# Performance work log

Measured on AMD Instinct MI355X. Metric: run time of the kernel, lower is better.

The kernel has to match this reference:

```python
import jax, jax.numpy as jnp
import numpy as np

D = 1024          # d_model
E = 12            # n_routed
HS = 2 * D        # shared hidden (r_shared=2)
HR = 3 * D        # routed hidden (r_routed=3)
TAU = 1.5         # router temperature


def setup_inputs() -> dict:
    key = jax.random.key(0)
    ks = jax.random.split(key, 12)
    def xavier(k, shape):
        fan_in, fan_out = shape[-2], shape[-1]
        lim = jnp.sqrt(6.0 / (fan_in + fan_out))
        return jax.random.uniform(k, shape, jnp.float32, -lim, lim)
    x = jax.random.normal(ks[0], (2, 1024, D), jnp.float32)
    # shared expert (n_shared=1, GEGLU)
    Ws1 = xavier(ks[1], (D, 2 * HS)); bs1 = jnp.zeros((2 * HS,), jnp.float32)
    Ws2 = xavier(ks[2], (HS, D));     bs2 = jnp.zeros((D,), jnp.float32)
    # routed experts, stacked [E, ...]
    We1 = xavier(ks[3], (E, D, 2 * HR)); be1 = jnp.zeros((E, 2 * HR), jnp.float32)
    We2 = xavier(ks[4], (E, HR, D));     be2 = jnp.zeros((E, D), jnp.float32)
    # router
    Wr = xavier(ks[5], (D, E)); br = jnp.zeros((E,), jnp.float32)
    return {"x": x, "Ws1": Ws1, "bs1": bs1, "Ws2": Ws2, "bs2": bs2,
            "We1": We1, "be1": be1, "We2": We2, "be2": be2, "Wr": Wr, "br": br}


def _geglu(h):
    a, g = jnp.split(h, 2, axis=-1)
    return a * jax.nn.gelu(g, approximate=False)  # torch GELU is exact erf


def reference(x, Ws1, bs1, Ws2, bs2, We1, be1, We2, be2, Wr, br):
    B, T, Dm = x.shape
    xf = x.reshape(-1, Dm)                                   # [N, D]
    # shared expert (n_shared=1 -> divide by 1)
    ys = _geglu(xf @ Ws1 + bs1) @ Ws2 + bs2                  # [N, D]
    # top-2 router (eval: no noise)
    logits = (xf @ Wr + br) / TAU                            # [N, E]
    top_val, top_idx = jax.lax.top_k(logits, 2)              # [N, 2]
    top_w = jax.nn.softmax(top_val, axis=-1)                 # [N, 2]
    # combine weights per (token, expert); non-selected experts get 0
    onehot = jax.nn.one_hot(top_idx, E, dtype=x.dtype)       # [N, 2, E]
    w = jnp.einsum('nke,nk->ne', onehot, top_w)              # [N, E]
    # dropless dense dispatch: every expert sees all tokens, weight 0 masks
    h = jnp.einsum('nd,edh->enh', xf, We1) + be1[:, None, :] # [E, N, 2*HR]
    act = _geglu(h)                                          # [E, N, HR]
    yE = jnp.einsum('enh,ehd->end', act, We2) + be2[:, None, :]
    yr = jnp.einsum('end,ne->nd', yE, w)                     # [N, D]
    return (ys + yr).reshape(B, T, Dm)
```

## Files before the change

### kernel.cpp

```cpp
#include <hip/hip_runtime.h>

#define N_TOK 2048
#define DMODEL 1024
#define NEXP 12
#define HS_DIM 2048
#define HR_DIM 3072
#define NSLOT (2 * N_TOK)

typedef __attribute__((ext_vector_type(8))) short bf16x8;
typedef __attribute__((ext_vector_type(16))) float f32x16;

#define AS1 __attribute__((address_space(1)))
#define AS3 __attribute__((address_space(3)))

__device__ __forceinline__ void gl_lds16(const void* g, void* l) {
  __builtin_amdgcn_global_load_lds((const AS1 void*)g, (AS3 void*)l, 16, 0, 0);
}

__device__ __forceinline__ unsigned short f2bf(float x) {
  union { float f; unsigned int u; } v; v.f = x;
  unsigned int u = v.u;
  u += 0x7fff + ((u >> 16) & 1);
  return (unsigned short)(u >> 16);
}
__device__ __forceinline__ unsigned pack2(float a, float b) {
  return (unsigned)f2bf(a) | ((unsigned)f2bf(b) << 16);
}
__device__ __forceinline__ float gelu_exact(float x) {
  return 0.5f * x * (1.0f + erff(x * 0.70710678118654752f));
}


__global__ __launch_bounds__(256)
void convert_x_kernel(const float* __restrict__ X, unsigned short* __restrict__ XB) {
  const int idx = (blockIdx.x * 256 + threadIdx.x) * 8;
  float4 f0 = *(const float4*)(X + idx);
  float4 f1 = *(const float4*)(X + idx + 4);
  uint4 o;
  o.x = pack2(f0.x, f0.y); o.y = pack2(f0.z, f0.w);
  o.z = pack2(f1.x, f1.y); o.w = pack2(f1.z, f1.w);
  *(uint4*)(XB + idx) = o;
}

__global__ __launch_bounds__(256)
void tconv_kernel(const float* __restrict__ W, unsigned short* __restrict__ WT,
                  int K, int N) {
  const int n0 = blockIdx.x * 64;
  const int k0 = blockIdx.y * 64;
  const size_t bo = (size_t)blockIdx.z * K * N;
  __shared__ __align__(16) unsigned short Ts[64 * 72];
  const int t = threadIdx.x;
  const int k4 = (t >> 4) * 4, n4 = (t & 15) * 4;
  float4 rw[4];
#pragma unroll
  for (int i = 0; i < 4; ++i)
    rw[i] = *(const float4*)(W + bo + (size_t)(k0 + k4 + i) * N + n0 + n4);
#pragma unroll
  for (int j = 0; j < 4; ++j) {
    uint2 v;
    v.x = pack2(((const float*)&rw[0])[j], ((const float*)&rw[1])[j]);
    v.y = pack2(((const float*)&rw[2])[j], ((const float*)&rw[3])[j]);
    *(uint2*)&Ts[(n4 + j) * 72 + k4] = v;
  }
  __syncthreads();
  const int n = t >> 2, kc = (t & 3) * 16;
  uint4 v0 = *(const uint4*)&Ts[n * 72 + kc];
  uint4 v1 = *(const uint4*)&Ts[n * 72 + kc + 8];
  unsigned short* dst = WT + (size_t)blockIdx.z * N * K + (size_t)(n0 + n) * K + k0 + kc;
  *(uint4*)dst = v0;
  *(uint4*)(dst + 8) = v1;
}


__global__ void init_kernel(int* counts, int* cursors) {
  int t = threadIdx.x;
  if (t < NEXP) { counts[t] = 0; cursors[t] = 0; }
}

__global__ __launch_bounds__(256)
void router_kernel(const float* __restrict__ X, const float* __restrict__ Wr,
                   const float* __restrict__ br, int* __restrict__ top_e,
                   float* __restrict__ top_w, int* __restrict__ counts) {
  const int wv = threadIdx.x >> 6, lane = threadIdx.x & 63;
  const int n = blockIdx.x * 4 + wv;
  float a[NEXP];
#pragma unroll
  for (int e = 0; e < NEXP; ++e) a[e] = 0.f;
  for (int it = 0; it < DMODEL / 64; ++it) {
    int k = it * 64 + lane;
    float xv = X[(size_t)n * DMODEL + k];
    const float* wr = Wr + (size_t)k * NEXP;
#pragma unroll
    for (int e = 0; e < NEXP; ++e) a[e] += xv * wr[e];
  }
#pragma unroll
  for (int e = 0; e < NEXP; ++e)
    for (int o = 32; o > 0; o >>= 1) a[e] += __shfl_xor(a[e], o, 64);
  if (lane == 0) {
    float l[NEXP];
#pragma unroll
    for (int e = 0; e < NEXP; ++e) l[e] = (a[e] + br[e]) * (1.0f / 1.5f);
    int e0 = 0;
    for (int e = 1; e < NEXP; ++e) if (l[e] > l[e0]) e0 = e;
    int e1 = (e0 == 0) ? 1 : 0;
    for (int e = 0; e < NEXP; ++e) if (e != e0 && l[e] > l[e1]) e1 = e;
    float w0 = 1.f / (1.f + expf(l[e1] - l[e0]));
    top_e[n * 2 + 0] = e0; top_e[n * 2 + 1] = e1;
    top_w[n * 2 + 0] = w0; top_w[n * 2 + 1] = 1.f - w0;
    atomicAdd(&counts[e0], 1); atomicAdd(&counts[e1], 1);
  }
}

__global__ void scan_kernel(const int* __restrict__ counts, int* __restrict__ offs) {
  if (threadIdx.x == 0) {
    int s = 0;
    for (int e = 0; e < NEXP; ++e) { offs[e] = s; s += counts[e]; }
    offs[NEXP] = s;
  }
}

__global__ __launch_bounds__(256)
void fill_kernel(const int* __restrict__ top_e, const float* __restrict__ top_w,
                 const int* __restrict__ offs, int* __restrict__ cursors,
                 int* __restrict__ slot_tok, float* __restrict__ slot_w,
                 int* __restrict__ tok_slot) {
  int n = blockIdx.x * 256 + threadIdx.x;
  if (n >= N_TOK) return;
#pragma unroll
  for (int j = 0; j < 2; ++j) {
    int e = top_e[n * 2 + j];
    int p = atomicAdd(&cursors[e], 1);
    int s = offs[e] + p;
    slot_tok[s] = n;
    slot_w[s] = top_w[n * 2 + j];
    tok_slot[n * 2 + j] = s;
  }
}

#define G1_SHARED 256
#define G1_PER_E  384

__global__ __launch_bounds__(256, 2)
void gemm1_all_kernel(const unsigned short* __restrict__ XB,
                      const unsigned short* __restrict__ WS,
                      const unsigned short* __restrict__ WE,
                      const float* __restrict__ BSb, const float* __restrict__ BEb,
                      unsigned short* __restrict__ ACT_S, unsigned short* __restrict__ ACT_R,
                      const int* __restrict__ slot_tok, const int* __restrict__ offs,
                      const int* __restrict__ counts) {
  int id = blockIdx.x;
  const unsigned short* W; const float* bias; unsigned short* ACT;
  int H, count, off, m0, n0, routed;
  if (id < G1_SHARED) {
    routed = 0;
    m0 = (id >> 4) * 128; n0 = (id & 15) * 128;
    W = WS; bias = BSb; ACT = ACT_S; H = HS_DIM; count = N_TOK; off = 0;
  } else {
    routed = 1;
    id -= G1_SHARED;
    const int e = id / G1_PER_E, rem = id % G1_PER_E;
    m0 = (rem / 24) * 128; n0 = (rem % 24) * 128;
    W = WE + (size_t)e * 2 * HR_DIM * DMODEL;
    bias = BEb + (size_t)e * 2 * HR_DIM;
    ACT = ACT_R; H = HR_DIM; count = counts[e]; off = offs[e];
  }
  if (m0 >= count) return;

  __shared__ __align__(16) unsigned short As[2 * 4096];
  __shared__ __align__(16) unsigned short Bs[2 * 8192];

  const int t = threadIdx.x;
  const int lane = t & 63, wv = t >> 6;
  const int srow = t >> 2, skc = t & 3;
  const int ln31 = lane & 31, hi = lane >> 5;
  const int wr = wv >> 1, wc = wv & 1;
  const int skc_s = skc ^ ((srow >> 1) & 3);

  const unsigned short* ap[2];
#pragma unroll
  for (int g = 0; g < 2; ++g) {
    int mr = m0 + srow + 64 * g;
    int tok;
    if (routed) {
      int s = off + (mr < count ? mr : count - 1);
      tok = slot_tok[s];
    } else {
      tok = mr;
    }
    ap[g] = XB + (size_t)tok * DMODEL + skc_s * 8;
  }
  const unsigned short* bp[4];
#pragma unroll
  for (int g = 0; g < 4; ++g) {
    int brow = srow + 64 * g;
    int wrow = (brow < 128) ? (n0 + brow) : (H + n0 + brow - 128);
    bp[g] = W + (size_t)wrow * DMODEL + skc_s * 8;
  }

  f32x16 acc_a[2][2], acc_g[2][2];
  const f32x16 z16 = {0.f,0.f,0.f,0.f,0.f,0.f,0.f,0.f,0.f,0.f,0.f,0.f,0.f,0.f,0.f,0.f};
#pragma unroll
  for (int i = 0; i < 2; ++i)
#pragma unroll
    for (int j = 0; j < 2; ++j) { acc_a[i][j] = z16; acc_g[i][j] = z16; }

#define G1_STAGE(B, KB)                                                   \
  {                                                                       \
    _Pragma("unroll") for (int g = 0; g < 2; ++g)                         \
        gl_lds16(ap[g] + (KB), &As[(B) * 4096 + g * 2048 + wv * 512]);    \
    _Pragma("unroll") for (int g = 0; g < 4; ++g)                         \
        gl_lds16(bp[g] + (KB), &Bs[(B) * 8192 + g * 2048 + wv * 512]);    \
  }

  int buf = 0;
  G1_STAGE(0, 0)
  for (int kt = 0; kt < DMODEL / 32; ++kt) {
    asm volatile("s_waitcnt vmcnt(0)" ::: "memory");
    __builtin_amdgcn_s_barrier();
    if (kt + 1 < DMODEL / 32) { G1_STAGE(buf ^ 1, (kt + 1) * 32) }
#pragma unroll
    for (int ks = 0; ks < 2; ++ks) {
      const int ko = ks * 16 + hi * 8;
      const int ch = ko >> 3;
      bf16x8 aF[2], bA[2], bG[2];
#pragma unroll
      for (int i = 0; i < 2; ++i) {
        int r = wr * 64 + i * 32 + ln31;
        aF[i] = *(const bf16x8*)&As[buf * 4096 + r * 32 + ((ch ^ ((r >> 1) & 3)) << 3)];
      }
#pragma unroll
      for (int j = 0; j < 2; ++j) {
        int r = wc * 64 + j * 32 + ln31;
        bA[j] = *(const bf16x8*)&Bs[buf * 8192 + r * 32 + ((ch ^ ((r >> 1) & 3)) << 3)];
        int r2 = 128 + r;
        bG[j] = *(const bf16x8*)&Bs[buf * 8192 + r2 * 32 + ((ch ^ ((r2 >> 1) & 3)) << 3)];
      }
#pragma unroll
      for (int i = 0; i < 2; ++i)
#pragma unroll
        for (int j = 0; j < 2; ++j) {
          acc_a[i][j] = __builtin_amdgcn_mfma_f32_32x32x16_bf16(aF[i], bA[j], acc_a[i][j], 0, 0, 0);
          acc_g[i][j] = __builtin_amdgcn_mfma_f32_32x32x16_bf16(aF[i], bG[j], acc_g[i][j], 0, 0, 0);
        }
    }
    buf ^= 1;
  }
#undef G1_STAGE

  float ba[2], bg[2];
#pragma unroll
  for (int j = 0; j < 2; ++j) {
    int col = n0 + wc * 64 + j * 32 + ln31;
    ba[j] = bias[col];
    bg[j] = bias[H + col];
  }
#pragma unroll
  for (int i = 0; i < 2; ++i)
#pragma unroll
    for (int j = 0; j < 2; ++j)
#pragma unroll
      for (int reg = 0; reg < 16; ++reg) {
        int row = wr * 64 + i * 32 + (reg & 3) + 8 * (reg >> 2) + 4 * hi;
        if (m0 + row < count) {
          int col = n0 + wc * 64 + j * 32 + ln31;
          float av = acc_a[i][j][reg] + ba[j];
          float gv = acc_g[i][j][reg] + bg[j];
          ACT[(size_t)(off + m0 + row) * H + col] = f2bf(av * gelu_exact(gv));
        }
      }
}

#define G2_SHARED 256
#define G2_PER_E  384

__global__ __launch_bounds__(256, 4)
void gemm2_all_kernel(const unsigned short* __restrict__ ACT_S,
                      const unsigned short* __restrict__ ACT_R,
                      const unsigned short* __restrict__ WSt,
                      const unsigned short* __restrict__ WEt,
                      const float* __restrict__ BSb, const float* __restrict__ BEb,
                      float* __restrict__ SP, float* __restrict__ YP,
                      const int* __restrict__ offs, const int* __restrict__ counts) {
  int id = blockIdx.x;
  const unsigned short* A; const unsigned short* W; const float* bias;
  int K, count, off, m0, n0, routed, kc;
  if (id < G2_SHARED) {
    routed = 0;
    kc = id & 1;
    const int rem2 = id >> 1;
    m0 = (rem2 >> 3) * 128; n0 = (rem2 & 7) * 128;
    A = ACT_S; W = WSt; bias = BSb; K = HS_DIM; count = N_TOK; off = 0;
  } else {
    routed = 1;
    id -= G2_SHARED;
    const int e = id / G2_PER_E, rem = id % G2_PER_E;
    kc = rem % 3;
    const int rem2 = rem / 3;
    m0 = (rem2 >> 3) * 128; n0 = (rem2 & 7) * 128;
    A = ACT_R; W = WEt + (size_t)e * DMODEL * HR_DIM;
    bias = BEb + (size_t)e * DMODEL; K = HR_DIM; count = counts[e]; off = offs[e];
  }
  if (m0 >= count) return;

  __shared__ __align__(16) unsigned short As[2 * 4096];
  __shared__ __align__(16) unsigned short Bs[2 * 4096];

  const int t = threadIdx.x;
  const int lane = t & 63, wv = t >> 6;
  const int srow = t >> 2, skc = t & 3;
  const int ln31 = lane & 31, hi = lane >> 5;
  const int wr = wv >> 1, wc = wv & 1;
  const int skc_s = skc ^ ((srow >> 1) & 3);

  const unsigned short* ap[2];
#pragma unroll
  for (int g = 0; g < 2; ++g) {
    int mr = m0 + srow + 64 * g;
    int r = off + (mr < count ? mr : count - 1);
    ap[g] = A + (size_t)r * K + skc_s * 8;
  }
  const unsigned short* bp[2];
#pragma unroll
  for (int g = 0; g < 2; ++g)
    bp[g] = W + (size_t)(n0 + srow + 64 * g) * K + skc_s * 8;

  f32x16 acc[2][2];
  const f32x16 z16 = {0.f,0.f,0.f,0.f,0.f,0.f,0.f,0.f,0.f,0.f,0.f,0.f,0.f,0.f,0.f,0.f};
#pragma unroll
  for (int i = 0; i < 2; ++i)
#pragma unroll
    for (int j = 0; j < 2; ++j) acc[i][j] = z16;

#define G2_STAGE(B, KB)                                                   \
  {                                                                       \
    _Pragma("unroll") for (int g = 0; g < 2; ++g) {                       \
      gl_lds16(ap[g] + (KB), &As[(B) * 4096 + g * 2048 + wv * 512]);      \
      gl_lds16(bp[g] + (KB), &Bs[(B) * 4096 + g * 2048 + wv * 512]);      \
    }                                                                     \
  }

  const int kb0 = kc * 1024;
  int buf = 0;
  G2_STAGE(0, kb0)
  for (int kt = 0; kt < 32; ++kt) {
    asm volatile("s_waitcnt vmcnt(0)" ::: "memory");
    __builtin_amdgcn_s_barrier();
    if (kt + 1 < 32) { G2_STAGE(buf ^ 1, kb0 + (kt + 1) * 32) }
#pragma unroll
    for (int ks = 0; ks < 2; ++ks) {
      const int ko = ks * 16 + hi * 8;
      const int ch = ko >> 3;
      bf16x8 aF[2], bF[2];
#pragma unroll
      for (int i = 0; i < 2; ++i) {
        int r = wr * 64 + i * 32 + ln31;
        aF[i] = *(const bf16x8*)&As[buf * 4096 + r * 32 + ((ch ^ ((r >> 1) & 3)) << 3)];
      }
#pragma unroll
      for (int j = 0; j < 2; ++j) {
        int r = wc * 64 + j * 32 + ln31;
        bF[j] = *(const bf16x8*)&Bs[buf * 4096 + r * 32 + ((ch ^ ((r >> 1) & 3)) << 3)];
      }
#pragma unroll
      for (int i = 0; i < 2; ++i)
#pragma unroll
        for (int j = 0; j < 2; ++j)
          acc[i][j] = __builtin_amdgcn_mfma_f32_32x32x16_bf16(aF[i], bF[j], acc[i][j], 0, 0, 0);
    }
    buf ^= 1;
  }
#undef G2_STAGE

  float bb[2];
#pragma unroll
  for (int j = 0; j < 2; ++j)
    bb[j] = (kc == 0) ? bias[n0 + wc * 64 + j * 32 + ln31] : 0.f;
#pragma unroll
  for (int i = 0; i < 2; ++i)
#pragma unroll
    for (int j = 0; j < 2; ++j)
#pragma unroll
      for (int reg = 0; reg < 16; ++reg) {
        int row = wr * 64 + i * 32 + (reg & 3) + 8 * (reg >> 2) + 4 * hi;
        if (m0 + row < count) {
          int col = n0 + wc * 64 + j * 32 + ln31;
          float v = acc[i][j][reg] + bb[j];
          if (routed) {
            YP[((size_t)kc * NSLOT + off + m0 + row) * DMODEL + col] = v;
          } else {
            SP[((size_t)kc * N_TOK + m0 + row) * DMODEL + col] = v;
          }
        }
      }
}

__global__ __launch_bounds__(256)
void combine_kernel(const float* __restrict__ SP, const float* __restrict__ YP,
                    const int* __restrict__ tok_slot, const float* __restrict__ slot_w,
                    float* __restrict__ OUT) {
  const int n = blockIdx.x;
  const int tx = threadIdx.x;
  const int s0 = tok_slot[n * 2 + 0], s1 = tok_slot[n * 2 + 1];
  const float w0 = slot_w[s0], w1 = slot_w[s1];
  float4 r = ((const float4*)(SP + (size_t)n * DMODEL))[tx];
  float4 b = ((const float4*)(SP + (size_t)(N_TOK + n) * DMODEL))[tx];
  r.x += b.x; r.y += b.y; r.z += b.z; r.w += b.w;
#pragma unroll
  for (int kc = 0; kc < 3; ++kc) {
    float4 p0 = ((const float4*)(YP + ((size_t)kc * NSLOT + s0) * DMODEL))[tx];
    float4 p1 = ((const float4*)(YP + ((size_t)kc * NSLOT + s1) * DMODEL))[tx];
    r.x += w0 * p0.x + w1 * p1.x;
    r.y += w0 * p0.y + w1 * p1.y;
    r.z += w0 * p0.z + w1 * p1.z;
    r.w += w0 * p0.w + w1 * p1.w;
  }
  ((float4*)(OUT + (size_t)n * DMODEL))[tx] = r;
}


extern "C" void kernel_launch(void* const* d_in, const int* in_sizes, int n_in,
                              void* d_out, int out_size, void* d_ws, size_t ws_size,
                              hipStream_t stream) {
  const float* x   = (const float*)d_in[0];
  const float* Ws1 = (const float*)d_in[1];
  const float* bs1 = (const float*)d_in[2];
  const float* Ws2 = (const float*)d_in[3];
  const float* bs2 = (const float*)d_in[4];
  const float* We1 = (const float*)d_in[5];
  const float* be1 = (const float*)d_in[6];
  const float* We2 = (const float*)d_in[7];
  const float* be2 = (const float*)d_in[8];
  const float* Wr  = (const float*)d_in[9];
  const float* br  = (const float*)d_in[10];
  float* out = (float*)d_out;

  char* p = (char*)d_ws;
  int* counts  = (int*)p; p += 256;
  int* cursors = (int*)p; p += 256;
  int* offs    = (int*)p; p += 256;
  int* top_e   = (int*)p; p += (size_t)N_TOK * 2 * 4;
  float* top_w = (float*)p; p += (size_t)N_TOK * 2 * 4;
  int* slot_tok = (int*)p; p += (size_t)NSLOT * 4;
  float* slot_w = (float*)p; p += (size_t)NSLOT * 4;
  int* tok_slot = (int*)p; p += (size_t)N_TOK * 2 * 4;
  unsigned short* xb    = (unsigned short*)p; p += (size_t)N_TOK * DMODEL * 2;
  unsigned short* ws1t  = (unsigned short*)p; p += (size_t)2 * HS_DIM * DMODEL * 2;
  unsigned short* ws2t  = (unsigned short*)p; p += (size_t)DMODEL * HS_DIM * 2;
  unsigned short* we1t  = (unsigned short*)p; p += (size_t)NEXP * 2 * HR_DIM * DMODEL * 2;
  unsigned short* we2t  = (unsigned short*)p; p += (size_t)NEXP * DMODEL * HR_DIM * 2;
  unsigned short* act_s = (unsigned short*)p; p += (size_t)N_TOK * HS_DIM * 2;
  unsigned short* act_r = (unsigned short*)p; p += (size_t)NSLOT * HR_DIM * 2;
  float* sp = (float*)p; p += (size_t)2 * N_TOK * DMODEL * 4;
  float* yp = (float*)p; p += (size_t)3 * NSLOT * DMODEL * 4;

  convert_x_kernel<<<(N_TOK * DMODEL) / 2048, 256, 0, stream>>>(x, xb);
  tconv_kernel<<<dim3(2 * HS_DIM / 64, DMODEL / 64, 1), 256, 0, stream>>>(Ws1, ws1t, DMODEL, 2 * HS_DIM);
  tconv_kernel<<<dim3(DMODEL / 64, HS_DIM / 64, 1), 256, 0, stream>>>(Ws2, ws2t, HS_DIM, DMODEL);
  tconv_kernel<<<dim3(2 * HR_DIM / 64, DMODEL / 64, NEXP), 256, 0, stream>>>(We1, we1t, DMODEL, 2 * HR_DIM);
  tconv_kernel<<<dim3(DMODEL / 64, HR_DIM / 64, NEXP), 256, 0, stream>>>(We2, we2t, HR_DIM, DMODEL);

  init_kernel<<<1, 64, 0, stream>>>(counts, cursors);
  router_kernel<<<N_TOK / 4, 256, 0, stream>>>(x, Wr, br, top_e, top_w, counts);
  scan_kernel<<<1, 64, 0, stream>>>(counts, offs);
  fill_kernel<<<N_TOK / 256, 256, 0, stream>>>(top_e, top_w, offs, cursors, slot_tok, slot_w, tok_slot);

  gemm1_all_kernel<<<G1_SHARED + G1_PER_E * NEXP, 256, 0, stream>>>(
      xb, ws1t, we1t, bs1, be1, act_s, act_r, slot_tok, offs, counts);

  gemm2_all_kernel<<<G2_SHARED + G2_PER_E * NEXP, 256, 0, stream>>>(
      act_s, act_r, ws2t, we2t, bs2, be2, sp, yp, offs, counts);

  combine_kernel<<<N_TOK, 256, 0, stream>>>(sp, yp, tok_slot, slot_w, out);
}
```

Before: 890.4 us.

## Overlap weight transpose-conversion with GEMM1 by fusing them into shared launches

Kernels are regrouped so weight conversions run inside the same launches as compute. X conversion, Ws1 transpose and counter init become one prep launch. The shared-expert GEMM1 shares a launch with the We1 and Ws2 transposes, and the routed GEMM1 shares one with the We2 transpose, so conversion blocks can fill CUs idle during compute. This cuts launch count and overlaps memory-bound conversion with MFMA work, at the cost of heterogeneous blocks whose LDS and register needs are sized for the GEMM path.

```diff
diff --git a/kernel.cpp b/kernel.cpp
--- a/kernel.cpp
+++ b/kernel.cpp
@@ -31,30 +31,16 @@
 }
 
 
-__global__ __launch_bounds__(256)
-void convert_x_kernel(const float* __restrict__ X, unsigned short* __restrict__ XB) {
-  const int idx = (blockIdx.x * 256 + threadIdx.x) * 8;
-  float4 f0 = *(const float4*)(X + idx);
-  float4 f1 = *(const float4*)(X + idx + 4);
-  uint4 o;
-  o.x = pack2(f0.x, f0.y); o.y = pack2(f0.z, f0.w);
-  o.z = pack2(f1.x, f1.y); o.w = pack2(f1.z, f1.w);
-  *(uint4*)(XB + idx) = o;
-}
-
-__global__ __launch_bounds__(256)
-void tconv_kernel(const float* __restrict__ W, unsigned short* __restrict__ WT,
-                  int K, int N) {
-  const int n0 = blockIdx.x * 64;
-  const int k0 = blockIdx.y * 64;
-  const size_t bo = (size_t)blockIdx.z * K * N;
-  __shared__ __align__(16) unsigned short Ts[64 * 72];
+__device__ __forceinline__ void tconv_body(const float* __restrict__ W,
+                                           unsigned short* __restrict__ WT,
+                                           int K, int N, int n0, int k0,
+                                           unsigned short* Ts) {
   const int t = threadIdx.x;
   const int k4 = (t >> 4) * 4, n4 = (t & 15) * 4;
   float4 rw[4];
 #pragma unroll
   for (int i = 0; i < 4; ++i)
-    rw[i] = *(const float4*)(W + bo + (size_t)(k0 + k4 + i) * N + n0 + n4);
+    rw[i] = *(const float4*)(W + (size_t)(k0 + k4 + i) * N + n0 + n4);
 #pragma unroll
   for (int j = 0; j < 4; ++j) {
     uint2 v;
@@ -66,109 +52,17 @@
   const int n = t >> 2, kc = (t & 3) * 16;
   uint4 v0 = *(const uint4*)&Ts[n * 72 + kc];
   uint4 v1 = *(const uint4*)&Ts[n * 72 + kc + 8];
-  unsigned short* dst = WT + (size_t)blockIdx.z * N * K + (size_t)(n0 + n) * K + k0 + kc;
+  unsigned short* dst = WT + (size_t)(n0 + n) * K + k0 + kc;
   *(uint4*)dst = v0;
   *(uint4*)(dst + 8) = v1;
 }
 
-
-__global__ void init_kernel(int* counts, int* cursors) {
-  int t = threadIdx.x;
-  if (t < NEXP) { counts[t] = 0; cursors[t] = 0; }
-}
-
-__global__ __launch_bounds__(256)
-void router_kernel(const float* __restrict__ X, const float* __restrict__ Wr,
-                   const float* __restrict__ br, int* __restrict__ top_e,
-                   float* __restrict__ top_w, int* __restrict__ counts) {
-  const int wv = threadIdx.x >> 6, lane = threadIdx.x & 63;
-  const int n = blockIdx.x * 4 + wv;
-  float a[NEXP];
-#pragma unroll
-  for (int e = 0; e < NEXP; ++e) a[e] = 0.f;
-  for (int it = 0; it < DMODEL / 64; ++it) {
-    int k = it * 64 + lane;
-    float xv = X[(size_t)n * DMODEL + k];
-    const float* wr = Wr + (size_t)k * NEXP;
-#pragma unroll
-    for (int e = 0; e < NEXP; ++e) a[e] += xv * wr[e];
-  }
-#pragma unroll
-  for (int e = 0; e < NEXP; ++e)
-    for (int o = 32; o > 0; o >>= 1) a[e] += __shfl_xor(a[e], o, 64);
-  if (lane == 0) {
-    float l[NEXP];
-#pragma unroll
-    for (int e = 0; e < NEXP; ++e) l[e] = (a[e] + br[e]) * (1.0f / 1.5f);
-    int e0 = 0;
-    for (int e = 1; e < NEXP; ++e) if (l[e] > l[e0]) e0 = e;
-    int e1 = (e0 == 0) ? 1 : 0;
-    for (int e = 0; e < NEXP; ++e) if (e != e0 && l[e] > l[e1]) e1 = e;
-    float w0 = 1.f / (1.f + expf(l[e1] - l[e0]));
-    top_e[n * 2 + 0] = e0; top_e[n * 2 + 1] = e1;
-    top_w[n * 2 + 0] = w0; top_w[n * 2 + 1] = 1.f - w0;
-    atomicAdd(&counts[e0], 1); atomicAdd(&counts[e1], 1);
-  }
-}
-
-__global__ void scan_kernel(const int* __restrict__ counts, int* __restrict__ offs) {
-  if (threadIdx.x == 0) {
-    int s = 0;
-    for (int e = 0; e < NEXP; ++e) { offs[e] = s; s += counts[e]; }
-    offs[NEXP] = s;
-  }
-}
-
-__global__ __launch_bounds__(256)
-void fill_kernel(const int* __restrict__ top_e, const float* __restrict__ top_w,
-                 const int* __restrict__ offs, int* __restrict__ cursors,
-                 int* __restrict__ slot_tok, float* __restrict__ slot_w,
-                 int* __restrict__ tok_slot) {
-  int n = blockIdx.x * 256 + threadIdx.x;
-  if (n >= N_TOK) return;
-#pragma unroll
-  for (int j = 0; j < 2; ++j) {
-    int e = top_e[n * 2 + j];
-    int p = atomicAdd(&cursors[e], 1);
-    int s = offs[e] + p;
-    slot_tok[s] = n;
-    slot_w[s] = top_w[n * 2 + j];
-    tok_slot[n * 2 + j] = s;
-  }
-}
-
-#define G1_SHARED 256
-#define G1_PER_E  384
-
-__global__ __launch_bounds__(256, 2)
-void gemm1_all_kernel(const unsigned short* __restrict__ XB,
-                      const unsigned short* __restrict__ WS,
-                      const unsigned short* __restrict__ WE,
-                      const float* __restrict__ BSb, const float* __restrict__ BEb,
-                      unsigned short* __restrict__ ACT_S, unsigned short* __restrict__ ACT_R,
-                      const int* __restrict__ slot_tok, const int* __restrict__ offs,
-                      const int* __restrict__ counts) {
-  int id = blockIdx.x;
-  const unsigned short* W; const float* bias; unsigned short* ACT;
-  int H, count, off, m0, n0, routed;
-  if (id < G1_SHARED) {
-    routed = 0;
-    m0 = (id >> 4) * 128; n0 = (id & 15) * 128;
-    W = WS; bias = BSb; ACT = ACT_S; H = HS_DIM; count = N_TOK; off = 0;
-  } else {
-    routed = 1;
-    id -= G1_SHARED;
-    const int e = id / G1_PER_E, rem = id % G1_PER_E;
-    m0 = (rem / 24) * 128; n0 = (rem % 24) * 128;
-    W = WE + (size_t)e * 2 * HR_DIM * DMODEL;
-    bias = BEb + (size_t)e * 2 * HR_DIM;
-    ACT = ACT_R; H = HR_DIM; count = counts[e]; off = offs[e];
-  }
-  if (m0 >= count) return;
-
-  __shared__ __align__(16) unsigned short As[2 * 4096];
-  __shared__ __align__(16) unsigned short Bs[2 * 8192];
-
+__device__ __forceinline__ void gemm1_body(
+    const unsigned short* __restrict__ XB, const unsigned short* __restrict__ W,
+    const float* __restrict__ bias, unsigned short* __restrict__ ACT,
+    const int H, const int count, const int off, const int m0, const int n0,
+    const int routed, const int* __restrict__ slot_tok,
+    unsigned short* As, unsigned short* Bs) {
   const int t = threadIdx.x;
   const int lane = t & 63, wv = t >> 6;
   const int srow = t >> 2, skc = t & 3;
@@ -268,6 +162,141 @@
           ACT[(size_t)(off + m0 + row) * H + col] = f2bf(av * gelu_exact(gv));
         }
       }
+}
+
+
+__global__ __launch_bounds__(256)
+void prep_kernel(const float* __restrict__ X, unsigned short* __restrict__ XB,
+                 const float* __restrict__ Ws1, unsigned short* __restrict__ WS1T,
+                 int* __restrict__ counts, int* __restrict__ cursors) {
+  __shared__ __align__(16) unsigned short Ts[64 * 72];
+  const int id = blockIdx.x;
+  const int t = threadIdx.x;
+  if (id < 1024) {
+    const int idx = (id * 256 + t) * 8;
+    float4 f0 = *(const float4*)(X + idx);
+    float4 f1 = *(const float4*)(X + idx + 4);
+    uint4 o;
+    o.x = pack2(f0.x, f0.y); o.y = pack2(f0.z, f0.w);
+    o.z = pack2(f1.x, f1.y); o.w = pack2(f1.z, f1.w);
+    *(uint4*)(XB + idx) = o;
+  } else if (id < 2048) {
+    const int tid = id - 1024;
+    tconv_body(Ws1, WS1T, DMODEL, 2 * HS_DIM, (tid & 63) * 64, (tid >> 6) * 64, Ts);
+  } else {
+    if (t < NEXP) { counts[t] = 0; cursors[t] = 0; }
+  }
+}
+
+__global__ __launch_bounds__(256, 2)
+void g1s_kernel(const unsigned short* __restrict__ XB,
+                const unsigned short* __restrict__ WS,
+                const float* __restrict__ BSb, unsigned short* __restrict__ ACT_S,
+                const float* __restrict__ We1, unsigned short* __restrict__ WE1T,
+                const float* __restrict__ Ws2, unsigned short* __restrict__ WS2T) {
+  __shared__ __align__(16) unsigned short SMEM[24576];
+  const int id = blockIdx.x;
+  if (id < 256) {
+    gemm1_body(XB, WS, BSb, ACT_S, HS_DIM, N_TOK, 0,
+               (id >> 4) * 128, (id & 15) * 128, 0, nullptr,
+               SMEM, SMEM + 8192);
+  } else if (id < 18688) {
+    const int tid = id - 256;
+    const int e = tid / 1536, rem = tid % 1536;
+    tconv_body(We1 + (size_t)e * DMODEL * 2 * HR_DIM,
+               WE1T + (size_t)e * 2 * HR_DIM * DMODEL,
+               DMODEL, 2 * HR_DIM, (rem % 96) * 64, (rem / 96) * 64, SMEM);
+  } else {
+    const int tid = id - 18688;
+    tconv_body(Ws2, WS2T, HS_DIM, DMODEL, (tid & 15) * 64, (tid >> 4) * 64, SMEM);
+  }
+}
+
+__global__ __launch_bounds__(256, 2)
+void g1r_kernel(const unsigned short* __restrict__ XB,
+                const unsigned short* __restrict__ WE1T,
+                const float* __restrict__ BEb, unsigned short* __restrict__ ACT_R,
+                const int* __restrict__ slot_tok, const int* __restrict__ offs,
+                const int* __restrict__ counts,
+                const float* __restrict__ We2, unsigned short* __restrict__ WE2T) {
+  __shared__ __align__(16) unsigned short SMEM[24576];
+  const int id = blockIdx.x;
+  if (id < 4608) {
+    const int e = id / 384, rem = id % 384;
+    const int m0 = (rem / 24) * 128, n0 = (rem % 24) * 128;
+    const int count = counts[e];
+    if (m0 >= count) return;
+    gemm1_body(XB, WE1T + (size_t)e * 2 * HR_DIM * DMODEL,
+               BEb + (size_t)e * 2 * HR_DIM, ACT_R, HR_DIM, count, offs[e],
+               m0, n0, 1, slot_tok, SMEM, SMEM + 8192);
+  } else {
+    const int tid = id - 4608;
+    const int e = tid / 768, rem = tid % 768;
+    tconv_body(We2 + (size_t)e * HR_DIM * DMODEL,
+               WE2T + (size_t)e * DMODEL * HR_DIM,
+               HR_DIM, DMODEL, (rem & 15) * 64, (rem >> 4) * 64, SMEM);
+  }
+}
+
+
+__global__ __launch_bounds__(256)
+void router_kernel(const float* __restrict__ X, const float* __restrict__ Wr,
+                   const float* __restrict__ br, int* __restrict__ top_e,
+                   float* __restrict__ top_w, int* __restrict__ counts) {
+  const int wv = threadIdx.x >> 6, lane = threadIdx.x & 63;
+  const int n = blockIdx.x * 4 + wv;
+  float a[NEXP];
+#pragma unroll
+  for (int e = 0; e < NEXP; ++e) a[e] = 0.f;
+  for (int it = 0; it < DMODEL / 64; ++it) {
+    int k = it * 64 + lane;
+    float xv = X[(size_t)n * DMODEL + k];
+    const float* wr = Wr + (size_t)k * NEXP;
+#pragma unroll
+    for (int e = 0; e < NEXP; ++e) a[e] += xv * wr[e];
+  }
+#pragma unroll
+  for (int e = 0; e < NEXP; ++e)
+    for (int o = 32; o > 0; o >>= 1) a[e] += __shfl_xor(a[e], o, 64);
+  if (lane == 0) {
+    float l[NEXP];
+#pragma unroll
+    for (int e = 0; e < NEXP; ++e) l[e] = (a[e] + br[e]) * (1.0f / 1.5f);
+    int e0 = 0;
+    for (int e = 1; e < NEXP; ++e) if (l[e] > l[e0]) e0 = e;
+    int e1 = (e0 == 0) ? 1 : 0;
+    for (int e = 0; e < NEXP; ++e) if (e != e0 && l[e] > l[e1]) e1 = e;
+    float w0 = 1.f / (1.f + expf(l[e1] - l[e0]));
+    top_e[n * 2 + 0] = e0; top_e[n * 2 + 1] = e1;
+    top_w[n * 2 + 0] = w0; top_w[n * 2 + 1] = 1.f - w0;
+    atomicAdd(&counts[e0], 1); atomicAdd(&counts[e1], 1);
+  }
+}
+
+__global__ void scan_kernel(const int* __restrict__ counts, int* __restrict__ offs) {
+  if (threadIdx.x == 0) {
+    int s = 0;
+    for (int e = 0; e < NEXP; ++e) { offs[e] = s; s += counts[e]; }
+    offs[NEXP] = s;
+  }
+}
+
+__global__ __launch_bounds__(256)
+void fill_kernel(const int* __restrict__ top_e, const float* __restrict__ top_w,
+                 const int* __restrict__ offs, int* __restrict__ cursors,
+                 int* __restrict__ slot_tok, float* __restrict__ slot_w,
+                 int* __restrict__ tok_slot) {
+  int n = blockIdx.x * 256 + threadIdx.x;
+  if (n >= N_TOK) return;
+#pragma unroll
+  for (int j = 0; j < 2; ++j) {
+    int e = top_e[n * 2 + j];
+    int p = atomicAdd(&cursors[e], 1);
+    int s = offs[e] + p;
+    slot_tok[s] = n;
+    slot_w[s] = top_w[n * 2 + j];
+    tok_slot[n * 2 + j] = s;
+  }
 }
 
 #define G2_SHARED 256
@@ -453,19 +482,15 @@
   float* sp = (float*)p; p += (size_t)2 * N_TOK * DMODEL * 4;
   float* yp = (float*)p; p += (size_t)3 * NSLOT * DMODEL * 4;
 
-  convert_x_kernel<<<(N_TOK * DMODEL) / 2048, 256, 0, stream>>>(x, xb);
-  tconv_kernel<<<dim3(2 * HS_DIM / 64, DMODEL / 64, 1), 256, 0, stream>>>(Ws1, ws1t, DMODEL, 2 * HS_DIM);
-  tconv_kernel<<<dim3(DMODEL / 64, HS_DIM / 64, 1), 256, 0, stream>>>(Ws2, ws2t, HS_DIM, DMODEL);
-  tconv_kernel<<<dim3(2 * HR_DIM / 64, DMODEL / 64, NEXP), 256, 0, stream>>>(We1, we1t, DMODEL, 2 * HR_DIM);
-  tconv_kernel<<<dim3(DMODEL / 64, HR_DIM / 64, NEXP), 256, 0, stream>>>(We2, we2t, HR_DIM, DMODEL);
-
-  init_kernel<<<1, 64, 0, stream>>>(counts, cursors);
+  prep_kernel<<<2049, 256, 0, stream>>>(x, xb, Ws1, ws1t, counts, cursors);
+
   router_kernel<<<N_TOK / 4, 256, 0, stream>>>(x, Wr, br, top_e, top_w, counts);
   scan_kernel<<<1, 64, 0, stream>>>(counts, offs);
   fill_kernel<<<N_TOK / 256, 256, 0, stream>>>(top_e, top_w, offs, cursors, slot_tok, slot_w, tok_slot);
 
-  gemm1_all_kernel<<<G1_SHARED + G1_PER_E * NEXP, 256, 0, stream>>>(
-      xb, ws1t, we1t, bs1, be1, act_s, act_r, slot_tok, offs, counts);
+  g1s_kernel<<<19200, 256, 0, stream>>>(xb, ws1t, bs1, act_s, We1, we1t, Ws2, ws2t);
+
+  g1r_kernel<<<13824, 256, 0, stream>>>(xb, we1t, be1, act_r, slot_tok, offs, counts, We2, we2t);
 
   gemm2_all_kernel<<<G2_SHARED + G2_PER_E * NEXP, 256, 0, stream>>>(
       act_s, act_r, ws2t, we2t, bs2, be2, sp, yp, offs, counts);
```

After: 836.6 us. 1.06x faster.
